# Kernel tuning notes

Measured on AMD Instinct MI355X. Metric: run time of the kernel, lower is better.

The kernel has to match this reference:

```python
import jax, jax.numpy as jnp
import numpy as np
import math

B, S, D, H = 2, 2048, 512, 8  # batch, seq, d_hidden (= per-head dim here), n_heads


def _rope(x):
    # x: [B, H, S, D]; standard interleaved RoPE with base 10000
    b, h, s, d = x.shape
    inv_freq = 1.0 / (10000.0 ** (jnp.arange(0, d, 2, dtype=jnp.float32) / d))  # [d/2]
    ang = jnp.arange(s, dtype=jnp.float32)[:, None] * inv_freq[None, :]          # [S, d/2]
    cos, sin = jnp.cos(ang), jnp.sin(ang)
    x1, x2 = x[..., 0::2], x[..., 1::2]
    r1 = x1 * cos - x2 * sin
    r2 = x1 * sin + x2 * cos
    return jnp.stack([r1, r2], axis=-1).reshape(b, h, s, d).astype(x.dtype)


def setup_inputs() -> dict:
    key = jax.random.key(0)
    kq, k1, k2, k3, k4 = jax.random.split(key, 5)
    std = 0.02
    return {
        "q": jax.random.normal(kq, (B, S, D), dtype=jnp.float32),
        "W_q": jax.random.normal(k1, (H, D, D), dtype=jnp.float32) * std,
        "W_k": jax.random.normal(k2, (H, D, D), dtype=jnp.float32) * std,
        "W_v": jax.random.normal(k3, (H, D, D), dtype=jnp.float32) * std,
        "W_o": jax.random.normal(k4, (H * D, D), dtype=jnp.float32) * std,
    }


def reference(q, W_q, W_k, W_v, W_o):
    b, s, d = q.shape
    h = W_q.shape[0]
    scale = 1.0 / math.sqrt(d)
    qh = jnp.einsum('bsz,hzd->bhsd', q, W_q)
    kh = jnp.einsum('bsz,hzd->bhsd', q, W_k)
    vh = jnp.einsum('bsz,hzd->bhsd', q, W_v)
    qh = _rope(qh)
    kh = _rope(kh)
    scores = jnp.einsum('bhqd,bhkd->bhqk', qh, kh) * scale
    causal = jnp.triu(jnp.ones((s, s), dtype=bool), k=1)  # True above diagonal
    scores = jnp.where(causal, -jnp.inf, scores)
    probs = jax.nn.softmax(scores, axis=-1)  # dropout is identity in eval
    # NOTE: faithful to the original (transposed) einsum: contracts over the
    # query index z of probs with the sequence index z of v.
    out = jnp.einsum('bhzs,bhzd->bhsd', probs, vh)
    out = out.transpose(0, 2, 1, 3).reshape(b, s, h * d)
    return jnp.einsum('bsz,zd->bsd', out, W_o)
```

## Files before the change

kernel.cpp:

```cpp
#include <hip/hip_runtime.h>
#include <hip/hip_bf16.h>
#include <math.h>
#include <stdint.h>

#define BB 2
#define SS 2048
#define DD 512
#define HH 8
#define NTOK (BB*SS)
#define NQKV (3*HH*DD)
#define BHD  (HH*DD)
#define NBH  (BB*HH)
#define NTILE 136

typedef __attribute__((ext_vector_type(8))) short short8v;
typedef __attribute__((ext_vector_type(4))) float floatx4;

__device__ __forceinline__ unsigned short f2bf(float f) {
  unsigned int u = __builtin_bit_cast(unsigned int, f);
  u = (u + 0x7FFFu + ((u >> 16) & 1u)) >> 16;
  return (unsigned short)u;
}
__device__ __forceinline__ float bf2f(unsigned short s) {
  unsigned int u = ((unsigned int)s) << 16;
  return __builtin_bit_cast(float, u);
}
__device__ __forceinline__ void async16(const void* g, void* l) {
  __builtin_amdgcn_global_load_lds(
      (const __attribute__((address_space(1))) unsigned int*)g,
      (__attribute__((address_space(3))) unsigned int*)l, 16, 0, 0);
}

__global__ __launch_bounds__(256)
void k_prep(const float* __restrict__ q,
            const float* __restrict__ Wq, const float* __restrict__ Wk,
            const float* __restrict__ Wv, const float* __restrict__ Wo,
            unsigned short* __restrict__ qbf, float* __restrict__ rope,
            unsigned short* __restrict__ Wcat, unsigned short* __restrict__ Wot,
            float* __restrict__ lsum, float* __restrict__ outz) {
  __shared__ float t[32][33];
  const int bid = blockIdx.x;
  const int tid = threadIdx.x;
  if (bid < 2048) {
    const int i = (bid * 256 + tid) * 4;
    const float4 v = *(const float4*)&q[i];
    ushort4 o;
    o.x = f2bf(v.x); o.y = f2bf(v.y); o.z = f2bf(v.z); o.w = f2bf(v.w);
    *(ushort4*)&qbf[i] = o;
  } else if (bid < 4096) {
    const int idx = (bid - 2048) * 256 + tid;
    const int dp = idx >> 11, s = idx & 2047;
    const float inv = exp2f(-13.287712379549449f * (1.0f/256.0f) * (float)dp);
    float sn, cs;
    __sincosf((float)s * inv, &sn, &cs);
    rope[(size_t)idx * 2]     = cs;
    rope[(size_t)idx * 2 + 1] = sn;
  } else if (bid < 12288) {
    const int flat = bid - 4096;
    const int bxi = flat & 15, byi = (flat >> 4) & 15, z = flat >> 8;
    const float* in; unsigned short* out; int inLD, outLD;
    float sc = 1.0f;
    if (z < 24) {
      int tsel = z / 8, h = z % 8;
      const float* w = (tsel == 0) ? Wq : (tsel == 1) ? Wk : Wv;
      if (tsel == 0) sc = 0.044194173824159216f;
      in = w + (size_t)h * DD * DD;
      out = Wcat + ((size_t)tsel * BHD + (size_t)h * DD) * DD;
      inLD = DD; outLD = DD;
    } else {
      int k = z - 24;
      in = Wo + (size_t)k * DD * DD;
      out = Wot + (size_t)k * DD;
      inLD = DD; outLD = BHD;
    }
    const int tx = tid & 31, ty = tid >> 5;
    const int bx = bxi * 32, by = byi * 32;
    for (int kk = 0; kk < 4; ++kk)
      t[ty + 8*kk][tx] = in[(size_t)(by + ty + 8*kk) * inLD + bx + tx];
    __syncthreads();
    for (int kk = 0; kk < 4; ++kk)
      out[(size_t)(bx + ty + 8*kk) * outLD + by + tx] = f2bf(t[tx][ty + 8*kk] * sc);
  } else if (bid < 12416) {
    lsum[(bid - 12288) * 256 + tid] = 0.0f;
  } else {
    const int i = ((bid - 12416) * 256 + tid) * 4;
    float4 zz; zz.x = 0.f; zz.y = 0.f; zz.z = 0.f; zz.w = 0.f;
    *(float4*)&outz[i] = zz;
  }
}

__global__ __launch_bounds__(256, 2)
void k_qkv(const unsigned short* __restrict__ Abf, const unsigned short* __restrict__ Bt,
           const float* __restrict__ rope,
           unsigned short* __restrict__ Qr, unsigned short* __restrict__ Kr,
           unsigned short* __restrict__ Vt) {
  __shared__ short As[128*32];
  __shared__ short Bs[256*32];
  const int tid = threadIdx.x;
  const int m0 = blockIdx.x * 128;
  const int n0 = blockIdx.y * 256;
  const int wave = tid >> 6, lane = tid & 63, qd = lane >> 4, c = lane & 15;
  const int wm = (wave >> 1) * 64, wn = (wave & 1) * 128;
  floatx4 acc[4][8] = {};
  const int e0 = tid * 8;
  const int r0 = e0 >> 5, c0 = e0 & 31;
  for (int k0 = 0; k0 < 512; k0 += 32) {
    __syncthreads();
    async16(&Abf[(size_t)(m0 + r0      ) * 512 + k0 + c0], &As[e0]);
    async16(&Abf[(size_t)(m0 + r0 +  64) * 512 + k0 + c0], &As[e0 + 2048]);
    async16(&Bt [(size_t)(n0 + r0      ) * 512 + k0 + c0], &Bs[e0]);
    async16(&Bt [(size_t)(n0 + r0 +  64) * 512 + k0 + c0], &Bs[e0 + 2048]);
    async16(&Bt [(size_t)(n0 + r0 + 128) * 512 + k0 + c0], &Bs[e0 + 4096]);
    async16(&Bt [(size_t)(n0 + r0 + 192) * 512 + k0 + c0], &Bs[e0 + 6144]);
    __syncthreads();
    short8v a[4], bfr[8];
    for (int mt = 0; mt < 4; ++mt) a[mt]   = *(const short8v*)&As[(wm + mt*16 + c)*32 + qd*8];
    for (int nt = 0; nt < 8; ++nt) bfr[nt] = *(const short8v*)&Bs[(wn + nt*16 + c)*32 + qd*8];
    for (int mt = 0; mt < 4; ++mt)
      for (int nt = 0; nt < 8; ++nt)
        acc[mt][nt] = __builtin_amdgcn_mfma_f32_16x16x32_bf16(a[mt], bfr[nt], acc[mt][nt], 0, 0, 0);
  }
  const int tsel = n0 >> 12;
  const int h = (n0 >> 9) & 7;
  const int bat = m0 >> 11;
  const int bh = bat * HH + h;
  const int dloc = (n0 & 511) + wn;
  if (tsel < 2) {
    unsigned short* dst = (tsel == 0) ? Qr : Kr;
    for (int nt = 0; nt < 8; ++nt) {
      const int d = dloc + nt*16 + c;
      const unsigned int sgn = (d & 1) ? 0u : 0x80000000u;
      const size_t rb = (size_t)(d >> 1) * (SS * 2);
      for (int mt = 0; mt < 4; ++mt) {
        const int mrow = (m0 & 2047) + wm + mt*16 + qd*4;
        const float4 t0 = *(const float4*)&rope[rb + (size_t)mrow * 2];
        const float4 t1 = *(const float4*)&rope[rb + (size_t)mrow * 2 + 4];
        const float cs[4] = {t0.x, t0.z, t1.x, t1.z};
        const float sn[4] = {t0.y, t0.w, t1.y, t1.w};
        for (int r = 0; r < 4; ++r) {
          const float v = acc[mt][nt][r];
          float p = __shfl_xor(v, 1, 64);
          p = __builtin_bit_cast(float, __builtin_bit_cast(unsigned int, p) ^ sgn);
          const float res = fmaf(p, sn[r], v * cs[r]);
          dst[((size_t)bh * SS + mrow + r) * DD + d] = f2bf(res);
        }
      }
    }
  } else {
    for (int nt = 0; nt < 8; ++nt) {
      const int d = dloc + nt*16 + c;
      const size_t vbase = ((size_t)bh * DD + d) * SS;
      for (int mt = 0; mt < 4; ++mt) {
        const int s = (m0 & 2047) + wm + mt*16 + qd*4;
        ushort4 u;
        u.x = f2bf(acc[mt][nt][0]); u.y = f2bf(acc[mt][nt][1]);
        u.z = f2bf(acc[mt][nt][2]); u.w = f2bf(acc[mt][nt][3]);
        *(ushort4*)&Vt[vbase + s] = u;
      }
    }
  }
}

__global__ __launch_bounds__(256)
void k_scores(const unsigned short* __restrict__ Qr, const unsigned short* __restrict__ Kr,
              unsigned short* __restrict__ Eg, float* __restrict__ lsum) {
  __shared__ short UN[17408];
  short* As0 = UN;
  short* As1 = UN + 4096;
  short* Bs0 = UN + 8192;
  short* Bs1 = UN + 12288;
  unsigned short* ET = (unsigned short*)UN;
  const int tid = threadIdx.x;
  const int bh = blockIdx.y;
  const int t = blockIdx.x;
  int zb = 0;
  while (((zb + 1) * (zb + 2)) / 2 <= t) ++zb;
  const int st = t - (zb * (zb + 1)) / 2;
  const int z0 = zb * 128, s0 = st * 128;
  const int wave = tid >> 6, lane = tid & 63, qd = lane >> 4, c = lane & 15;
  const int wm = (wave >> 1) * 64, wn = (wave & 1) * 64;
  const size_t qb = (size_t)bh * SS * DD;
  floatx4 acc[4][4] = {};
  const int e0 = tid * 8, e1 = e0 + 2048;
  const int r0 = e0 >> 5, c0 = e0 & 31, r1 = e1 >> 5, c1 = e1 & 31;
  for (int k0 = 0; k0 < 512; k0 += 64) {
    __syncthreads();
    async16(&Qr[qb + (size_t)(z0 + r0) * 512 + k0      + c0], &As0[e0]);
    async16(&Qr[qb + (size_t)(z0 + r1) * 512 + k0      + c1], &As0[e1]);
    async16(&Qr[qb + (size_t)(z0 + r0) * 512 + k0 + 32 + c0], &As1[e0]);
    async16(&Qr[qb + (size_t)(z0 + r1) * 512 + k0 + 32 + c1], &As1[e1]);
    async16(&Kr[qb + (size_t)(s0 + r0) * 512 + k0      + c0], &Bs0[e0]);
    async16(&Kr[qb + (size_t)(s0 + r1) * 512 + k0      + c1], &Bs0[e1]);
    async16(&Kr[qb + (size_t)(s0 + r0) * 512 + k0 + 32 + c0], &Bs1[e0]);
    async16(&Kr[qb + (size_t)(s0 + r1) * 512 + k0 + 32 + c1], &Bs1[e1]);
    __syncthreads();
    for (int kc = 0; kc < 2; ++kc) {
      const short* Asp = kc ? As1 : As0;
      const short* Bsp = kc ? Bs1 : Bs0;
      short8v a[4], bfr[4];
      for (int mt = 0; mt < 4; ++mt) a[mt]   = *(const short8v*)&Asp[(wm + mt*16 + c)*32 + qd*8];
      for (int nt = 0; nt < 4; ++nt) bfr[nt] = *(const short8v*)&Bsp[(wn + nt*16 + c)*32 + qd*8];
      for (int mt = 0; mt < 4; ++mt)
        for (int nt = 0; nt < 4; ++nt)
          acc[mt][nt] = __builtin_amdgcn_mfma_f32_16x16x32_bf16(a[mt], bfr[nt], acc[mt][nt], 0, 0, 0);
    }
  }
  const bool diag = (st == zb);
  for (int mt = 0; mt < 4; ++mt) {
    const int zl = wm + mt*16 + qd*4;
    float rs[4] = {0.f, 0.f, 0.f, 0.f};
    for (int nt = 0; nt < 4; ++nt) {
      const int sl = wn + nt*16 + c;
      for (int r = 0; r < 4; ++r) {
        float ev = __expf(acc[mt][nt][r]);
        if (diag && (sl > zl + r)) ev = 0.f;
        acc[mt][nt][r] = ev;
        rs[r] += ev;
      }
    }
    for (int off = 1; off < 16; off <<= 1)
      for (int r = 0; r < 4; ++r) rs[r] += __shfl_xor(rs[r], off, 64);
    if (c == 0)
      for (int r = 0; r < 4; ++r)
        atomicAdd(&lsum[(size_t)bh * SS + z0 + zl + r], rs[r]);
  }
  __syncthreads();
  for (int mt = 0; mt < 4; ++mt) {
    const int zl = wm + mt*16 + qd*4;
    for (int nt = 0; nt < 4; ++nt) {
      const int sl = wn + nt*16 + c;
      ushort4 u;
      u.x = f2bf(acc[mt][nt][0]); u.y = f2bf(acc[mt][nt][1]);
      u.z = f2bf(acc[mt][nt][2]); u.w = f2bf(acc[mt][nt][3]);
      *(ushort4*)&ET[sl * 136 + zl] = u;
    }
  }
  __syncthreads();
  const size_t tb = ((size_t)bh * NTILE + t) * 16384;
  for (int it = 0; it < 8; ++it) {
    const int e = it * 2048 + tid * 8;
    const int row = e >> 7, col = e & 127;
    *(short8v*)&Eg[tb + row * 128 + col] = *(const short8v*)&ET[row * 136 + col];
  }
}

__global__ void k_vscale(unsigned short* __restrict__ Vt, const float* __restrict__ lsum) {
  const int idx = (blockIdx.x * 256 + threadIdx.x) * 8;
  const int z = idx & (SS - 1);
  const int bh = idx >> 20;
  short8v v = *(const short8v*)&Vt[idx];
  const float* lp = &lsum[(size_t)bh * SS + z];
  short8v o;
  for (int i = 0; i < 8; ++i)
    o[i] = (short)f2bf(bf2f((unsigned short)v[i]) / lp[i]);
  *(short8v*)&Vt[idx] = o;
}

__global__ __launch_bounds__(256)
void k_pv(const unsigned short* __restrict__ Eg, const unsigned short* __restrict__ Vs,
          unsigned short* __restrict__ Ocat) {
  __shared__ short Vl[2][128*32];
  __shared__ short ElA[2][128*32];
  __shared__ short ElB[2][128*32];
  const int tid = threadIdx.x;
  const int d0 = blockIdx.x * 128;
  const int pr = blockIdx.y;
  const int bh = blockIdx.z;
  const int stA = pr, stB = 15 - pr;
  const int bat = bh >> 3, h = bh & 7;
  const int wave = tid >> 6, lane = tid & 63, qd = lane >> 4, c = lane & 15;
  const int wm = (wave >> 1) * 64, wn = (wave & 1) * 64;
  const size_t vbb = (size_t)bh * DD * SS;
  const int e = tid * 8;
  floatx4 accA[4][4] = {};
  floatx4 accB[4][4] = {};
  for (int zb = stA; zb < 16; ++zb) {
    const bool actB = (zb >= stB);
    const size_t tri = (size_t)bh * NTILE + (zb * (zb + 1)) / 2;
    const size_t tbA = (tri + stA) * 16384;
    const size_t tbB = (tri + stB) * 16384;
    for (int half = 0; half < 2; ++half) {
      const int zbase = zb * 128 + half * 64;
      __syncthreads();
      for (int i = 0; i < 4; ++i) {
        const int ee = e + i * 2048;
        const int kc = ee >> 12, row = (ee >> 5) & 127, col = ee & 31;
        async16(&Vs[vbb + (size_t)(d0 + row) * SS + zbase + kc * 32 + col], &Vl[kc][row * 32 + col]);
      }
      for (int i = 0; i < 4; ++i) {
        const int ee = e + i * 2048;
        const int kc = ee >> 12, row = (ee >> 5) & 127, col = ee & 31;
        async16(&Eg[tbA + (size_t)row * 128 + half * 64 + kc * 32 + col], &ElA[kc][row * 32 + col]);
      }
      if (actB)
        for (int i = 0; i < 4; ++i) {
          const int ee = e + i * 2048;
          const int kc = ee >> 12, row = (ee >> 5) & 127, col = ee & 31;
          async16(&Eg[tbB + (size_t)row * 128 + half * 64 + kc * 32 + col], &ElB[kc][row * 32 + col]);
        }
      __syncthreads();
      for (int kc = 0; kc < 2; ++kc) {
        short8v a[4], bA[4];
        for (int dt = 0; dt < 4; ++dt) a[dt] = *(const short8v*)&Vl[kc][(wm + dt*16 + c)*32 + qd*8];
        for (int nt = 0; nt < 4; ++nt) bA[nt] = *(const short8v*)&ElA[kc][(wn + nt*16 + c)*32 + qd*8];
        for (int dt = 0; dt < 4; ++dt)
          for (int nt = 0; nt < 4; ++nt)
            accA[dt][nt] = __builtin_amdgcn_mfma_f32_16x16x32_bf16(a[dt], bA[nt], accA[dt][nt], 0, 0, 0);
        if (actB) {
          short8v bB[4];
          for (int nt = 0; nt < 4; ++nt) bB[nt] = *(const short8v*)&ElB[kc][(wn + nt*16 + c)*32 + qd*8];
          for (int dt = 0; dt < 4; ++dt)
            for (int nt = 0; nt < 4; ++nt)
              accB[dt][nt] = __builtin_amdgcn_mfma_f32_16x16x32_bf16(a[dt], bB[nt], accB[dt][nt], 0, 0, 0);
        }
      }
    }
  }
  for (int sel = 0; sel < 2; ++sel) {
    const int s0 = (sel ? stB : stA) * 128;
    floatx4 (&acc)[4][4] = sel ? accB : accA;
    for (int nt = 0; nt < 4; ++nt) {
      const int sg = s0 + wn + nt*16 + c;
      const size_t ob = ((size_t)(bat * SS + sg)) * BHD + (size_t)h * DD + d0;
      for (int dt = 0; dt < 4; ++dt) {
        const int dloc = wm + dt*16 + qd*4;
        ushort4 u;
        u.x = f2bf(acc[dt][nt][0]); u.y = f2bf(acc[dt][nt][1]);
        u.z = f2bf(acc[dt][nt][2]); u.w = f2bf(acc[dt][nt][3]);
        *(ushort4*)&Ocat[ob + dloc] = u;
      }
    }
  }
}

__global__ __launch_bounds__(256)
void k_oproj(const unsigned short* __restrict__ Ocat, const unsigned short* __restrict__ Wot,
             float* __restrict__ out) {
  __shared__ short As[2][128*32];
  __shared__ short Bs[2][128*32];
  const int tid = threadIdx.x;
  const int m0 = blockIdx.x * 128;
  const int n0 = blockIdx.y * 128;
  const int ks = blockIdx.z * 1024;
  const int wave = tid >> 6, lane = tid & 63, qd = lane >> 4, c = lane & 15;
  const int wm = (wave >> 1) * 64, wn = (wave & 1) * 64;
  floatx4 acc[4][4] = {};
  const int e0 = tid * 8, e1 = e0 + 2048;
  const int r0 = e0 >> 5, c0 = e0 & 31, r1 = e1 >> 5, c1 = e1 & 31;
  for (int k0 = ks; k0 < ks + 1024; k0 += 64) {
    __syncthreads();
    for (int kc = 0; kc < 2; ++kc) {
      const int kk = k0 + kc * 32;
      async16(&Ocat[(size_t)(m0 + r0) * BHD + kk + c0], &As[kc][e0]);
      async16(&Ocat[(size_t)(m0 + r1) * BHD + kk + c1], &As[kc][e1]);
      async16(&Wot [(size_t)(n0 + r0) * BHD + kk + c0], &Bs[kc][e0]);
      async16(&Wot [(size_t)(n0 + r1) * BHD + kk + c1], &Bs[kc][e1]);
    }
    __syncthreads();
    for (int kc = 0; kc < 2; ++kc) {
      short8v a[4], b[4];
      for (int mt = 0; mt < 4; ++mt) a[mt] = *(const short8v*)&As[kc][(wm + mt*16 + c)*32 + qd*8];
      for (int nt = 0; nt < 4; ++nt) b[nt] = *(const short8v*)&Bs[kc][(wn + nt*16 + c)*32 + qd*8];
      for (int mt = 0; mt < 4; ++mt)
        for (int nt = 0; nt < 4; ++nt)
          acc[mt][nt] = __builtin_amdgcn_mfma_f32_16x16x32_bf16(a[mt], b[nt], acc[mt][nt], 0, 0, 0);
    }
  }
  for (int mt = 0; mt < 4; ++mt) {
    const int m = m0 + wm + mt*16 + qd*4;
    for (int nt = 0; nt < 4; ++nt) {
      const int n = n0 + wn + nt*16 + c;
      for (int r = 0; r < 4; ++r)
        atomicAdd(&out[(size_t)(m + r) * DD + n], acc[mt][nt][r]);
    }
  }
}

extern "C" void kernel_launch(void* const* d_in, const int* in_sizes, int n_in,
                              void* d_out, int out_size, void* d_ws, size_t ws_size,
                              hipStream_t stream) {
  const float* q  = (const float*)d_in[0];
  const float* Wq = (const float*)d_in[1];
  const float* Wk = (const float*)d_in[2];
  const float* Wv = (const float*)d_in[3];
  const float* Wo = (const float*)d_in[4];

  char* base = (char*)d_ws;
  unsigned short* Eg   = (unsigned short*)base;
  unsigned short* qbf  = (unsigned short*)base;
  unsigned short* Wcat = (unsigned short*)(base + 4194304);
  float*          rope = (float*)(base + 16777216);
  char* p = base + 71303168;
  unsigned short* Wot  = (unsigned short*)p; p += 4194304;
  unsigned short* Qr   = (unsigned short*)p;
  unsigned short* Ocat = (unsigned short*)p; p += 33554432;
  unsigned short* Kr   = (unsigned short*)p; p += 33554432;
  unsigned short* Vt   = (unsigned short*)p; p += 33554432;
  float*          lsum = (float*)p;

  k_prep<<<14464, 256, 0, stream>>>(q, Wq, Wk, Wv, Wo, qbf, rope, Wcat, Wot, lsum, (float*)d_out);
  k_qkv<<<dim3(32,48), 256, 0, stream>>>(qbf, Wcat, rope, Qr, Kr, Vt);
  k_scores<<<dim3(NTILE,16), 256, 0, stream>>>(Qr, Kr, Eg, lsum);
  k_vscale<<<NBH*DD*SS/(256*8), 256, 0, stream>>>(Vt, lsum);
  k_pv<<<dim3(4,8,16), 256, 0, stream>>>(Eg, Vt, Ocat);
  k_oproj<<<dim3(32,4,4), 256, 0, stream>>>(Ocat, Wot, (float*)d_out);
}
```

Baseline: 400.2 us.

## Widen score tiles to 128x256 and write exp scores directly to global

Each k_scores block now computes a 128x256 tile (two key tiles), so one Q tile load is shared across two K tiles. The grid changes to a 3D launch over key-pair, query-block and batch-head, and blocks entirely above the causal diagonal exit early. The K step shrinks to 32, and the LDS transpose staging pass is dropped in favour of direct ushort4 stores into the transposed Eg layout. The trade-off is more accumulator registers per thread (launch_bounds 256,2), masked work on the upper half of diagonal pairs, and less coalesced global stores.

After: 414.1 us. +3.5%, slower.

```diff
diff --git a/kernel.cpp b/kernel.cpp
--- a/kernel.cpp
+++ b/kernel.cpp
@@ -161,86 +161,67 @@
   }
 }
 
-__global__ __launch_bounds__(256)
+__global__ __launch_bounds__(256, 2)
 void k_scores(const unsigned short* __restrict__ Qr, const unsigned short* __restrict__ Kr,
               unsigned short* __restrict__ Eg, float* __restrict__ lsum) {
-  __shared__ short UN[17408];
-  short* As0 = UN;
-  short* As1 = UN + 4096;
-  short* Bs0 = UN + 8192;
-  short* Bs1 = UN + 12288;
-  unsigned short* ET = (unsigned short*)UN;
-  const int tid = threadIdx.x;
-  const int bh = blockIdx.y;
-  const int t = blockIdx.x;
-  int zb = 0;
-  while (((zb + 1) * (zb + 2)) / 2 <= t) ++zb;
-  const int st = t - (zb * (zb + 1)) / 2;
-  const int z0 = zb * 128, s0 = st * 128;
+  __shared__ short As[128*32];
+  __shared__ short Bs[256*32];
+  const int sp = blockIdx.x;
+  const int zb = blockIdx.y;
+  const int bh = blockIdx.z;
+  const int st0 = sp * 2;
+  if (st0 > zb) return;
+  const int z0 = zb * 128, s0 = sp * 256;
+  const int tid = threadIdx.x;
   const int wave = tid >> 6, lane = tid & 63, qd = lane >> 4, c = lane & 15;
-  const int wm = (wave >> 1) * 64, wn = (wave & 1) * 64;
+  const int wm = (wave >> 1) * 64, wn = (wave & 1) * 128;
   const size_t qb = (size_t)bh * SS * DD;
-  floatx4 acc[4][4] = {};
-  const int e0 = tid * 8, e1 = e0 + 2048;
-  const int r0 = e0 >> 5, c0 = e0 & 31, r1 = e1 >> 5, c1 = e1 & 31;
-  for (int k0 = 0; k0 < 512; k0 += 64) {
-    __syncthreads();
-    async16(&Qr[qb + (size_t)(z0 + r0) * 512 + k0      + c0], &As0[e0]);
-    async16(&Qr[qb + (size_t)(z0 + r1) * 512 + k0      + c1], &As0[e1]);
-    async16(&Qr[qb + (size_t)(z0 + r0) * 512 + k0 + 32 + c0], &As1[e0]);
-    async16(&Qr[qb + (size_t)(z0 + r1) * 512 + k0 + 32 + c1], &As1[e1]);
-    async16(&Kr[qb + (size_t)(s0 + r0) * 512 + k0      + c0], &Bs0[e0]);
-    async16(&Kr[qb + (size_t)(s0 + r1) * 512 + k0      + c1], &Bs0[e1]);
-    async16(&Kr[qb + (size_t)(s0 + r0) * 512 + k0 + 32 + c0], &Bs1[e0]);
-    async16(&Kr[qb + (size_t)(s0 + r1) * 512 + k0 + 32 + c1], &Bs1[e1]);
-    __syncthreads();
-    for (int kc = 0; kc < 2; ++kc) {
-      const short* Asp = kc ? As1 : As0;
-      const short* Bsp = kc ? Bs1 : Bs0;
-      short8v a[4], bfr[4];
-      for (int mt = 0; mt < 4; ++mt) a[mt]   = *(const short8v*)&Asp[(wm + mt*16 + c)*32 + qd*8];
-      for (int nt = 0; nt < 4; ++nt) bfr[nt] = *(const short8v*)&Bsp[(wn + nt*16 + c)*32 + qd*8];
-      for (int mt = 0; mt < 4; ++mt)
-        for (int nt = 0; nt < 4; ++nt)
-          acc[mt][nt] = __builtin_amdgcn_mfma_f32_16x16x32_bf16(a[mt], bfr[nt], acc[mt][nt], 0, 0, 0);
-    }
-  }
-  const bool diag = (st == zb);
+  floatx4 acc[4][8] = {};
+  const int e0 = tid * 8;
+  const int r0 = e0 >> 5, c0 = e0 & 31;
+  for (int k0 = 0; k0 < 512; k0 += 32) {
+    __syncthreads();
+    async16(&Qr[qb + (size_t)(z0 + r0      ) * 512 + k0 + c0], &As[e0]);
+    async16(&Qr[qb + (size_t)(z0 + r0 +  64) * 512 + k0 + c0], &As[e0 + 2048]);
+    async16(&Kr[qb + (size_t)(s0 + r0      ) * 512 + k0 + c0], &Bs[e0]);
+    async16(&Kr[qb + (size_t)(s0 + r0 +  64) * 512 + k0 + c0], &Bs[e0 + 2048]);
+    async16(&Kr[qb + (size_t)(s0 + r0 + 128) * 512 + k0 + c0], &Bs[e0 + 4096]);
+    async16(&Kr[qb + (size_t)(s0 + r0 + 192) * 512 + k0 + c0], &Bs[e0 + 6144]);
+    __syncthreads();
+    short8v a[4], bfr[8];
+    for (int mt = 0; mt < 4; ++mt) a[mt]   = *(const short8v*)&As[(wm + mt*16 + c)*32 + qd*8];
+    for (int nt = 0; nt < 8; ++nt) bfr[nt] = *(const short8v*)&Bs[(wn + nt*16 + c)*32 + qd*8];
+    for (int mt = 0; mt < 4; ++mt)
+      for (int nt = 0; nt < 8; ++nt)
+        acc[mt][nt] = __builtin_amdgcn_mfma_f32_16x16x32_bf16(a[mt], bfr[nt], acc[mt][nt], 0, 0, 0);
+  }
+  const size_t tbL = ((size_t)bh * NTILE + (zb * (zb + 1)) / 2 + st0) * 16384;
+  const size_t tbH = tbL + 16384;
+  const bool hiOK = (st0 < zb);
   for (int mt = 0; mt < 4; ++mt) {
     const int zl = wm + mt*16 + qd*4;
+    const int zg = z0 + zl;
     float rs[4] = {0.f, 0.f, 0.f, 0.f};
-    for (int nt = 0; nt < 4; ++nt) {
+    for (int nt = 0; nt < 8; ++nt) {
       const int sl = wn + nt*16 + c;
-      for (int r = 0; r < 4; ++r) {
-        float ev = __expf(acc[mt][nt][r]);
-        if (diag && (sl > zl + r)) ev = 0.f;
-        acc[mt][nt][r] = ev;
-        rs[r] += ev;
+      const int sg = s0 + sl;
+      const float ev0 = (sg <= zg + 0) ? __expf(acc[mt][nt][0]) : 0.f;
+      const float ev1 = (sg <= zg + 1) ? __expf(acc[mt][nt][1]) : 0.f;
+      const float ev2 = (sg <= zg + 2) ? __expf(acc[mt][nt][2]) : 0.f;
+      const float ev3 = (sg <= zg + 3) ? __expf(acc[mt][nt][3]) : 0.f;
+      rs[0] += ev0; rs[1] += ev1; rs[2] += ev2; rs[3] += ev3;
+      if (sl < 128 || hiOK) {
+        ushort4 u;
+        u.x = f2bf(ev0); u.y = f2bf(ev1); u.z = f2bf(ev2); u.w = f2bf(ev3);
+        const size_t tb = (sl < 128) ? tbL : tbH;
+        *(ushort4*)&Eg[tb + (size_t)(sl & 127) * 128 + zl] = u;
       }
     }
     for (int off = 1; off < 16; off <<= 1)
       for (int r = 0; r < 4; ++r) rs[r] += __shfl_xor(rs[r], off, 64);
     if (c == 0)
       for (int r = 0; r < 4; ++r)
-        atomicAdd(&lsum[(size_t)bh * SS + z0 + zl + r], rs[r]);
-  }
-  __syncthreads();
-  for (int mt = 0; mt < 4; ++mt) {
-    const int zl = wm + mt*16 + qd*4;
-    for (int nt = 0; nt < 4; ++nt) {
-      const int sl = wn + nt*16 + c;
-      ushort4 u;
-      u.x = f2bf(acc[mt][nt][0]); u.y = f2bf(acc[mt][nt][1]);
-      u.z = f2bf(acc[mt][nt][2]); u.w = f2bf(acc[mt][nt][3]);
-      *(ushort4*)&ET[sl * 136 + zl] = u;
-    }
-  }
-  __syncthreads();
-  const size_t tb = ((size_t)bh * NTILE + t) * 16384;
-  for (int it = 0; it < 8; ++it) {
-    const int e = it * 2048 + tid * 8;
-    const int row = e >> 7, col = e & 127;
-    *(short8v*)&Eg[tb + row * 128 + col] = *(const short8v*)&ET[row * 136 + col];
+        atomicAdd(&lsum[(size_t)bh * SS + zg + r], rs[r]);
   }
 }
 
@@ -400,7 +381,7 @@
 
   k_prep<<<14464, 256, 0, stream>>>(q, Wq, Wk, Wv, Wo, qbf, rope, Wcat, Wot, lsum, (float*)d_out);
   k_qkv<<<dim3(32,48), 256, 0, stream>>>(qbf, Wcat, rope, Qr, Kr, Vt);
-  k_scores<<<dim3(NTILE,16), 256, 0, stream>>>(Qr, Kr, Eg, lsum);
+  k_scores<<<dim3(8,16,16), 256, 0, stream>>>(Qr, Kr, Eg, lsum);
   k_vscale<<<NBH*DD*SS/(256*8), 256, 0, stream>>>(Vt, lsum);
   k_pv<<<dim3(4,8,16), 256, 0, stream>>>(Eg, Vt, Ocat);
   k_oproj<<<dim3(32,4,4), 256, 0, stream>>>(Ocat, Wot, (float*)d_out);
```
